# Optimization experiments

Measured on AMD Instinct MI355X. Metric: run time of the kernel, lower is better.

## Reference

```python
import jax, jax.numpy as jnp
import numpy as np
from jax import lax

T_DATA = 20000
E_NO = 2000
I_NO = 500
SUB_NO = 16
SYN_B = 3
HID = 256
T_SYN = 200
T_ENC = 80


def _causal_conv(x, kern):
    # x: [T, S] per-subunit drive; kern: [S, K] causal kernels (index = lag)
    S, K = kern.shape
    lhs = jnp.pad(x.T, ((0, 0), (K - 1, 0)))[None]        # [1, S, T+K-1]
    rhs = kern[:, ::-1][:, None, :]                        # flip then correlate == torch conv1d path
    out = lax.conv_general_dilated(lhs, rhs, (1,), 'VALID', feature_group_count=S)
    return out[0].T                                        # [T, S]


def setup_inputs() -> dict:
    key = jax.random.key(0)
    ks = jax.random.split(key, 16)
    V_in = jax.random.normal(ks[0], (T_DATA,), jnp.float32) * 5.0 - 69.0
    S_e = jax.random.bernoulli(ks[1], 0.02, (T_DATA, E_NO)).astype(jnp.float32)
    S_i = jax.random.bernoulli(ks[2], 0.02, (T_DATA, I_NO)).astype(jnp.float32)
    # synapse -> subunit one-hot assignment matrices [sub_no, n_syn]
    C_syn_e = jax.nn.one_hot(jax.random.randint(ks[3], (E_NO,), 0, SUB_NO), SUB_NO, dtype=jnp.float32).T
    C_syn_i = jax.nn.one_hot(jax.random.randint(ks[4], (I_NO,), 0, SUB_NO), SUB_NO, dtype=jnp.float32).T
    # parameters, initialized exactly as in __init__
    K_syn = jnp.stack([jnp.full((SUB_NO, SYN_B), 0.04),
                       jnp.full((SUB_NO, SYN_B), -0.02),
                       jnp.full((SUB_NO, SYN_B), 0.02)], axis=-1)          # [sub, B, 3]
    tau_syn = jnp.tile((jnp.arange(SYN_B, dtype=jnp.float32) + 1.6)[:, None], (1, 3))  # [B, 3]
    delta_syn = jnp.full((SUB_NO, 2), 2.0, jnp.float32)
    enc_bias = jnp.zeros((SUB_NO - 1,), jnp.float32)
    W_in = 2 * T_ENC - 1

    def lin(k, fan_out, fan_in):
        kw, kb = jax.random.split(k)
        s = 1.0 / np.sqrt(fan_in)
        return (jax.random.uniform(kw, (fan_out, fan_in), jnp.float32, -s, s),
                jax.random.uniform(kb, (fan_out,), jnp.float32, -s, s))

    W1, b1 = lin(ks[5], HID, W_in)
    W2, b2 = lin(ks[6], HID, HID)
    W3, b3 = lin(ks[7], HID, HID)
    W4, b4 = lin(ks[8], SUB_NO - 1, HID)
    a1 = jnp.float32(0.25)
    a2 = jnp.float32(0.25)
    a3 = jnp.float32(0.25)
    return dict(V_in=V_in, S_e=S_e, S_i=S_i, C_syn_e=C_syn_e, C_syn_i=C_syn_i,
                K_syn=K_syn, tau_syn=tau_syn, delta_syn=delta_syn, enc_bias=enc_bias,
                W1=W1, b1=b1, a1=a1, W2=W2, b2=b2, a2=a2, W3=W3, b3=b3, a3=a3,
                W4=W4, b4=b4)


def reference(V_in, S_e, S_i, C_syn_e, C_syn_i, K_syn, tau_syn, delta_syn, enc_bias,
              W1, b1, a1, W2, b2, a2, W3, b3, a3, W4, b4):
    T = V_in.shape[0]
    # ---- spike_convolve, fully vectorized over (subunit, basis) ----
    t = jnp.arange(T_SYN, dtype=V_in.dtype)                 # [T_syn]
    d = jnp.exp(delta_syn)                                   # [sub, 2]
    te = jnp.maximum(t[None, :] - d[:, 0:1], 0.0)            # [sub, T_syn]
    ti = jnp.maximum(t[None, :] - d[:, 1:2], 0.0)
    tau = jnp.exp(tau_syn)                                   # [B, 3]
    tte = te[:, None, :] / tau[None, :, 0, None]             # [sub, B, T_syn]
    tti = ti[:, None, :] / tau[None, :, 1, None]
    ker_e = jnp.einsum('sbt,sb->st', tte * jnp.exp(-tte), K_syn[:, :, 0])
    ker_i = jnp.einsum('sbt,sb->st', tti * jnp.exp(-tti), K_syn[:, :, 1])
    in_e = S_e @ C_syn_e.T                                   # [T, sub]
    in_i = S_i @ C_syn_i.T
    S_conv = _causal_conv(in_e, ker_e) + _causal_conv(in_i, ker_i)   # [T, sub]
    # ---- encode: batched sliding-window MLP (replaces per-timestep loop) ----
    W = 2 * T_ENC - 1
    Vpad = jnp.zeros((T + W,), V_in.dtype).at[T_ENC - 1:T_ENC - 1 + T].set(V_in)
    idx = jnp.arange(T)[:, None] + jnp.arange(W)[None, :]    # [T, W]
    win = Vpad[idx]                                          # [T, W]
    prelu = lambda x, a: jnp.where(x >= 0, x, a * x)
    h = prelu(win @ W1.T + b1, a1)
    h = prelu(h @ W2.T + b2, a2)
    h = prelu(h @ W3.T + b3, a3)
    nn_out = h @ W4.T + b4                                   # [T, sub-1]
    return jax.nn.sigmoid(nn_out + S_conv[:, 1:] + enc_bias)
```

## Files before the change

kernel.cpp:

```cpp
#include <hip/hip_runtime.h>
#include <cstdint>
#include <cstddef>

#define T_DATA 20000
#define E_NO 2000
#define I_NO 500
#define SUB_NO 16
#define HID 256
#define T_SYN 200
#define T_ENC 80
#define W_IN 159

typedef __attribute__((ext_vector_type(8))) __bf16 bf16x8;
typedef __attribute__((ext_vector_type(8))) short short8;
typedef __attribute__((ext_vector_type(4))) float floatx4;
typedef __attribute__((ext_vector_type(4))) unsigned int uint4v;
typedef __attribute__((ext_vector_type(2))) unsigned int uint2v;

__device__ __forceinline__ float bf2f(unsigned short u) {
    union { unsigned int i; float f; } v; v.i = ((unsigned int)u) << 16; return v.f;
}
__device__ __forceinline__ unsigned short f2bf(float f) {
    union { float f; unsigned int i; } v; v.f = f;
    unsigned int r = v.i + 0x7FFFu + ((v.i >> 16) & 1u);
    return (unsigned short)(r >> 16);
}
__device__ __forceinline__ float inload(const void* p, int i, int isbf) {
    return isbf ? bf2f(((const unsigned short*)p)[i]) : ((const float*)p)[i];
}

__device__ __forceinline__ int detect_bf(const void* Se, int* sfl) {
    if (threadIdx.x == 0) *sfl = 0;
    __syncthreads();
    const unsigned int* w = (const unsigned int*)Se;
    int la = 0;
    #pragma unroll
    for (int i = 0; i < 4; i++)
        la |= (w[i * 256 + threadIdx.x] & 0xFFFFu) ? 1 : 0;
    if (la) atomicOr(sfl, 1);
    __syncthreads();
    return *sfl;
}

#define OFF_KERE   16u
#define OFF_KERI   12816u
#define OFF_SHE    25616u
#define OFF_SHI    33616u
#define OFF_W1H    35616u
#define OFF_W1L    117536u
#define OFF_W2H    199456u
#define OFF_W2L    330528u
#define OFF_W3H    461600u
#define OFF_W3L    592672u
#define OFF_W4H    723744u
#define OFF_W4L    731424u
#define OFF_INE    739104u
#define OFF_INI    1059104u
#define OFF_SCONV  1379104u

__global__ void k_setup(const void* Se, const void* Ksyn, const void* tau_syn, const void* dly,
                        const void* Ce, const void* Ci,
                        const void* W1, const void* W2, const void* W3, const void* W4,
                        float* ker_e, float* ker_i, unsigned char* sh_e, unsigned char* sh_i,
                        unsigned short* W1h, unsigned short* W1l,
                        unsigned short* W2h, unsigned short* W2l,
                        unsigned short* W3h, unsigned short* W3l,
                        unsigned short* W4h, unsigned short* W4l) {
    __shared__ int sfl;
    int f = detect_bf(Se, &sfl);
    int id = blockIdx.x * 256 + threadIdx.x;
    if (id < 6400) {
        int c = id < 3200 ? 0 : 1;
        int q = id - c * 3200;
        int s = q / 200, j = q - s * 200;
        float d = expf(inload(dly, s * 2 + c, f));
        float tt = fmaxf((float)j - d, 0.0f);
        float acc = 0.f;
        #pragma unroll
        for (int b = 0; b < 3; b++) {
            float tau = expf(inload(tau_syn, b * 3 + c, f));
            float x = tt / tau;
            acc += x * expf(-x) * inload(Ksyn, (s * 3 + b) * 3 + c, f);
        }
        (c == 0 ? ker_e : ker_i)[s * 200 + j] = acc;
    } else if (id < 8400) {
        int e = id - 6400;
        int a = 0;
        for (int s = 0; s < 16; s++) if (inload(Ce, s * E_NO + e, f) > 0.5f) a = s;
        sh_e[e] = (unsigned char)(a * 8);
    } else if (id < 8900) {
        int e = id - 8400;
        int a = 0;
        for (int s = 0; s < 16; s++) if (inload(Ci, s * I_NO + e, f) > 0.5f) a = s;
        sh_i[e] = (unsigned char)(a * 8);
    } else if (id < 49860) {
        int q = id - 8900;
        int n = q / 160, k = q - n * 160;
        float v = (k < W_IN) ? inload(W1, n * W_IN + k, f) : 0.f;
        unsigned short hi = f2bf(v);
        W1h[q] = hi;
        W1l[q] = f2bf(v - bf2f(hi));
    } else if (id < 115396) {
        int q = id - 49860;
        float v = inload(W2, q, f);
        unsigned short hi = f2bf(v);
        W2h[q] = hi;
        W2l[q] = f2bf(v - bf2f(hi));
    } else if (id < 180932) {
        int q = id - 115396;
        float v = inload(W3, q, f);
        unsigned short hi = f2bf(v);
        W3h[q] = hi;
        W3l[q] = f2bf(v - bf2f(hi));
    } else if (id < 184772) {
        int q = id - 180932;
        float v = inload(W4, q, f);
        unsigned short hi = f2bf(v);
        W4h[q] = hi;
        W4l[q] = f2bf(v - bf2f(hi));
    }
}

__device__ __forceinline__ void acc_slot(unsigned int b, unsigned int sh,
                                         unsigned long long& lo, unsigned long long& hi) {
    unsigned int up = sh >> 6;
    unsigned int s6 = sh & 63;
    lo += (unsigned long long)(b & (up ^ 1u)) << s6;
    hi += (unsigned long long)(b & up) << s6;
}

__global__ void __launch_bounds__(256) k_spikes(const void* Se, const void* Si,
                         const unsigned char* sh_e, const unsigned char* sh_i,
                         unsigned char* in_e, unsigned char* in_i) {
    __shared__ int sfl;
    __shared__ __align__(8) unsigned char she[E_NO];
    __shared__ __align__(8) unsigned char shi[I_NO];
    for (int i = threadIdx.x; i < E_NO / 4; i += 256)
        ((unsigned int*)she)[i] = ((const unsigned int*)sh_e)[i];
    for (int i = threadIdx.x; i < I_NO / 4; i += 256)
        ((unsigned int*)shi)[i] = ((const unsigned int*)sh_i)[i];
    int f = detect_bf(Se, &sfl);
    int lane = threadIdx.x & 63;
    int wave = threadIdx.x >> 6;
    int t = blockIdx.x * 4 + wave;
    unsigned long long e0 = 0, e1 = 0, i0 = 0, i1 = 0;
    if (f) {
        const uint4v* re = (const uint4v*)((const unsigned short*)Se + (size_t)t * E_NO);
        #pragma unroll
        for (int it = 0; it < 4; it++) {
            int c = it * 64 + lane;
            if (c < 250) {
                uint4v v = re[c];
                unsigned long long q = *(const unsigned long long*)&she[c * 8];
                #pragma unroll
                for (int w = 0; w < 4; w++) {
                    unsigned int x = v[w];
                    acc_slot((x >> 7) & 1u,  (unsigned int)(q >> (16 * w)) & 0xFFu, e0, e1);
                    acc_slot((x >> 23) & 1u, (unsigned int)(q >> (16 * w + 8)) & 0xFFu, e0, e1);
                }
            }
        }
        const uint2v* ri = (const uint2v*)((const unsigned short*)Si + (size_t)t * I_NO);
        #pragma unroll
        for (int it = 0; it < 2; it++) {
            int c = it * 64 + lane;
            if (c < 125) {
                uint2v v = ri[c];
                unsigned int q = *(const unsigned int*)&shi[c * 4];
                #pragma unroll
                for (int w = 0; w < 2; w++) {
                    unsigned int x = v[w];
                    acc_slot((x >> 7) & 1u,  (q >> (16 * w)) & 0xFFu, i0, i1);
                    acc_slot((x >> 23) & 1u, (q >> (16 * w + 8)) & 0xFFu, i0, i1);
                }
            }
        }
    } else {
        const uint4v* re = (const uint4v*)((const float*)Se + (size_t)t * E_NO);
        #pragma unroll
        for (int it = 0; it < 8; it++) {
            int c = it * 64 + lane;
            if (c < 500) {
                uint4v v = re[c];
                unsigned int q = *(const unsigned int*)&she[c * 4];
                #pragma unroll
                for (int w = 0; w < 4; w++)
                    acc_slot((v[w] >> 23) & 1u, (q >> (8 * w)) & 0xFFu, e0, e1);
            }
        }
        const uint2v* ri = (const uint2v*)((const float*)Si + (size_t)t * I_NO);
        #pragma unroll
        for (int it = 0; it < 4; it++) {
            int c = it * 64 + lane;
            if (c < 250) {
                uint2v v = ri[c];
                unsigned int q = *(const unsigned short*)&shi[c * 2];
                #pragma unroll
                for (int w = 0; w < 2; w++)
                    acc_slot((v[w] >> 23) & 1u, (q >> (8 * w)) & 0xFFu, i0, i1);
            }
        }
    }
    for (int off = 32; off; off >>= 1) {
        e0 += __shfl_xor(e0, off);
        e1 += __shfl_xor(e1, off);
        i0 += __shfl_xor(i0, off);
        i1 += __shfl_xor(i1, off);
    }
    if (lane < 16) {
        unsigned long long a = (lane < 8) ? e0 : e1;
        in_e[(size_t)t * 16 + lane] = (unsigned char)((a >> ((lane & 7) * 8)) & 0xFF);
    } else if (lane < 32) {
        int s = lane - 16;
        unsigned long long a = (s < 8) ? i0 : i1;
        in_i[(size_t)t * 16 + s] = (unsigned char)((a >> ((s & 7) * 8)) & 0xFF);
    }
}

__global__ void __launch_bounds__(256) k_conv(
        const unsigned char* in_e, const unsigned char* in_i,
        const float* ker_e, const float* ker_i, float* S_conv) {
    __shared__ float se[263 * 17];
    __shared__ float si[263 * 17];
    __shared__ float ke[16 * 201];
    __shared__ float ki[16 * 201];
    int t0 = blockIdx.x * 64;
    for (int idx = threadIdx.x; idx < 263 * 4; idx += 256) {
        int r = idx >> 2, wi = idx & 3;
        int t = t0 - 199 + r;
        unsigned int ve = 0, vi = 0;
        if (t >= 0 && t < T_DATA) {
            ve = ((const unsigned int*)in_e)[t * 4 + wi];
            vi = ((const unsigned int*)in_i)[t * 4 + wi];
        }
        #pragma unroll
        for (int b = 0; b < 4; b++) {
            se[r * 17 + wi * 4 + b] = (float)((ve >> (8 * b)) & 0xFF);
            si[r * 17 + wi * 4 + b] = (float)((vi >> (8 * b)) & 0xFF);
        }
    }
    for (int idx = threadIdx.x; idx < 3200; idx += 256) {
        int s = idx / 200, j = idx - s * 200;
        ke[s * 201 + j] = ker_e[idx];
        ki[s * 201 + j] = ker_i[idx];
    }
    __syncthreads();
    int s = threadIdx.x & 15, g4 = (threadIdx.x >> 4) * 4;
    float a0 = 0.f, a1 = 0.f, a2 = 0.f, a3 = 0.f;
    float w0 = se[(g4 + 199) * 17 + s], w1 = se[(g4 + 200) * 17 + s];
    float w2 = se[(g4 + 201) * 17 + s], w3 = se[(g4 + 202) * 17 + s];
    float x0 = si[(g4 + 199) * 17 + s], x1 = si[(g4 + 200) * 17 + s];
    float x2 = si[(g4 + 201) * 17 + s], x3 = si[(g4 + 202) * 17 + s];
    #pragma unroll 4
    for (int j = 0; j < 200; j++) {
        float kej = ke[s * 201 + j];
        float kij = ki[s * 201 + j];
        a0 += w0 * kej + x0 * kij;
        a1 += w1 * kej + x1 * kij;
        a2 += w2 * kej + x2 * kij;
        a3 += w3 * kej + x3 * kij;
        int lr = g4 + 198 - j; lr = lr < 0 ? 0 : lr;
        float nw = se[lr * 17 + s], nx = si[lr * 17 + s];
        w3 = w2; w2 = w1; w1 = w0; w0 = nw;
        x3 = x2; x2 = x1; x1 = x0; x0 = nx;
    }
    int tb = t0 + g4;
    if (tb + 0 < T_DATA) S_conv[(size_t)(tb + 0) * 16 + s] = a0;
    if (tb + 1 < T_DATA) S_conv[(size_t)(tb + 1) * 16 + s] = a1;
    if (tb + 2 < T_DATA) S_conv[(size_t)(tb + 2) * 16 + s] = a2;
    if (tb + 3 < T_DATA) S_conv[(size_t)(tb + 3) * 16 + s] = a3;
}

template<bool BF>
__device__ __forceinline__ void mlp_body(
    const void* V,
    const unsigned short* W1h, const unsigned short* W1l, const void* b1, const void* a1p,
    const unsigned short* W2h, const unsigned short* W2l, const void* b2, const void* a2p,
    const unsigned short* W3h, const unsigned short* W3l, const void* b3, const void* a3p,
    const unsigned short* W4h, const unsigned short* W4l, const void* b4,
    const void* encb, const float* S_conv, void* out,
    unsigned short* Ahi, unsigned short* Alo)
{
    int tid = threadIdx.x;
    int lane = tid & 63, wave = tid >> 6;
    int lm = lane & 15, quad = lane >> 4;
    int t0 = blockIdx.x * 32;

    auto ld = [&](const void* p, int i) -> float {
        return BF ? bf2f(((const unsigned short*)p)[i]) : ((const float*)p)[i];
    };

    for (int idx = tid; idx < 32 * 160; idx += 256) {
        int m = idx / 160, k = idx - m * 160;
        int tg = t0 + m + k - (T_ENC - 1);
        float v = 0.f;
        if (k < W_IN && tg >= 0 && tg < T_DATA) v = ld(V, tg);
        unsigned short hi = f2bf(v);
        int col = (((k >> 3) ^ m) << 3) | (k & 7);
        Ahi[m * 256 + col] = hi;
        Alo[m * 256 + col] = f2bf(v - bf2f(hi));
    }
    __syncthreads();

    floatx4 acc[2][4];
    auto aoff = [&](int mt, int ks) {
        int arow = mt * 16 + lm;
        return arow * 256 + ((((ks << 2) | quad) ^ arow) << 3);
    };

    auto epi = [&](const void* bias, float alpha) {
        __syncthreads();
        #pragma unroll
        for (int mt = 0; mt < 2; mt++) {
            #pragma unroll
            for (int nt = 0; nt < 4; nt++) {
                int cn = wave * 64 + nt * 16 + lm;
                float bb = ld(bias, cn);
                #pragma unroll
                for (int j = 0; j < 4; j++) {
                    int row = mt * 16 + quad * 4 + j;
                    float h = acc[mt][nt][j] + bb;
                    h = (h >= 0.f) ? h : alpha * h;
                    unsigned short hi = f2bf(h);
                    int col = (((cn >> 3) ^ row) << 3) | (cn & 7);
                    Ahi[row * 256 + col] = hi;
                    Alo[row * 256 + col] = f2bf(h - bf2f(hi));
                }
            }
        }
        __syncthreads();
    };

    floatx4 z = {0.f, 0.f, 0.f, 0.f};
    {
        #pragma unroll
        for (int mt = 0; mt < 2; mt++)
            #pragma unroll
            for (int nt = 0; nt < 4; nt++) acc[mt][nt] = z;
        #pragma unroll
        for (int ks = 0; ks < 5; ks++) {
            bf16x8 ah0 = *(const bf16x8*)&Ahi[aoff(0, ks)];
            bf16x8 ah1 = *(const bf16x8*)&Ahi[aoff(1, ks)];
            bf16x8 al0, al1;
            if (!BF) { al0 = *(const bf16x8*)&Alo[aoff(0, ks)];
                       al1 = *(const bf16x8*)&Alo[aoff(1, ks)]; }
            #pragma unroll
            for (int nt = 0; nt < 4; nt++) {
                int cn = wave * 64 + nt * 16 + lm;
                size_t bo = (size_t)cn * 160 + ks * 32 + quad * 8;
                bf16x8 bh = *(const bf16x8*)(W1h + bo);
                acc[0][nt] = __builtin_amdgcn_mfma_f32_16x16x32_bf16(ah0, bh, acc[0][nt], 0, 0, 0);
                acc[1][nt] = __builtin_amdgcn_mfma_f32_16x16x32_bf16(ah1, bh, acc[1][nt], 0, 0, 0);
                if (!BF) {
                    bf16x8 bl = *(const bf16x8*)(W1l + bo);
                    acc[0][nt] = __builtin_amdgcn_mfma_f32_16x16x32_bf16(al0, bh, acc[0][nt], 0, 0, 0);
                    acc[1][nt] = __builtin_amdgcn_mfma_f32_16x16x32_bf16(al1, bh, acc[1][nt], 0, 0, 0);
                    acc[0][nt] = __builtin_amdgcn_mfma_f32_16x16x32_bf16(ah0, bl, acc[0][nt], 0, 0, 0);
                    acc[1][nt] = __builtin_amdgcn_mfma_f32_16x16x32_bf16(ah1, bl, acc[1][nt], 0, 0, 0);
                }
            }
        }
        epi(b1, ld(a1p, 0));
    }
    const unsigned short* Whs[2] = {W2h, W3h};
    const unsigned short* Wls[2] = {W2l, W3l};
    const void* bs[2] = {b2, b3};
    const void* as_[2] = {a2p, a3p};
    for (int l = 0; l < 2; l++) {
        #pragma unroll
        for (int mt = 0; mt < 2; mt++)
            #pragma unroll
            for (int nt = 0; nt < 4; nt++) acc[mt][nt] = z;
        const unsigned short* Wh = Whs[l];
        const unsigned short* Wl = Wls[l];
        #pragma unroll
        for (int ks = 0; ks < 8; ks++) {
            bf16x8 ah0 = *(const bf16x8*)&Ahi[aoff(0, ks)];
            bf16x8 ah1 = *(const bf16x8*)&Ahi[aoff(1, ks)];
            bf16x8 al0 = *(const bf16x8*)&Alo[aoff(0, ks)];
            bf16x8 al1 = *(const bf16x8*)&Alo[aoff(1, ks)];
            #pragma unroll
            for (int nt = 0; nt < 4; nt++) {
                int cn = wave * 64 + nt * 16 + lm;
                size_t bo = (size_t)cn * 256 + ks * 32 + quad * 8;
                bf16x8 bh = *(const bf16x8*)(Wh + bo);
                acc[0][nt] = __builtin_amdgcn_mfma_f32_16x16x32_bf16(ah0, bh, acc[0][nt], 0, 0, 0);
                acc[1][nt] = __builtin_amdgcn_mfma_f32_16x16x32_bf16(ah1, bh, acc[1][nt], 0, 0, 0);
                acc[0][nt] = __builtin_amdgcn_mfma_f32_16x16x32_bf16(al0, bh, acc[0][nt], 0, 0, 0);
                acc[1][nt] = __builtin_amdgcn_mfma_f32_16x16x32_bf16(al1, bh, acc[1][nt], 0, 0, 0);
                if (!BF) {
                    bf16x8 bl = *(const bf16x8*)(Wl + bo);
                    acc[0][nt] = __builtin_amdgcn_mfma_f32_16x16x32_bf16(ah0, bl, acc[0][nt], 0, 0, 0);
                    acc[1][nt] = __builtin_amdgcn_mfma_f32_16x16x32_bf16(ah1, bl, acc[1][nt], 0, 0, 0);
                }
            }
        }
        epi(bs[l], ld(as_[l], 0));
    }
    if (wave < 2) {
        int mt = wave;
        short8 z8 = {0, 0, 0, 0, 0, 0, 0, 0};
        bf16x8 bz = __builtin_bit_cast(bf16x8, z8);
        floatx4 a4 = z;
        #pragma unroll
        for (int ks = 0; ks < 8; ks++) {
            bf16x8 ah = *(const bf16x8*)&Ahi[aoff(mt, ks)];
            bf16x8 al = *(const bf16x8*)&Alo[aoff(mt, ks)];
            bf16x8 bh = bz, bl = bz;
            if (lm < 15) {
                size_t bo = (size_t)lm * 256 + ks * 32 + quad * 8;
                bh = *(const bf16x8*)(W4h + bo);
                if (!BF) bl = *(const bf16x8*)(W4l + bo);
            }
            a4 = __builtin_amdgcn_mfma_f32_16x16x32_bf16(ah, bh, a4, 0, 0, 0);
            a4 = __builtin_amdgcn_mfma_f32_16x16x32_bf16(al, bh, a4, 0, 0, 0);
            if (!BF)
                a4 = __builtin_amdgcn_mfma_f32_16x16x32_bf16(ah, bl, a4, 0, 0, 0);
        }
        if (lm < 15) {
            float bb = ld(b4, lm) + ld(encb, lm);
            #pragma unroll
            for (int j = 0; j < 4; j++) {
                int row = mt * 16 + quad * 4 + j;
                int t = t0 + row;
                float x = a4[j] + bb + S_conv[(size_t)t * 16 + lm + 1];
                x = fminf(fmaxf(x, -40.f), 40.f);
                float sg = 1.f / (1.f + expf(-x));
                if (BF) ((unsigned short*)out)[(size_t)t * 15 + lm] = f2bf(sg);
                else    ((float*)out)[(size_t)t * 15 + lm] = sg;
            }
        }
    }
}

__global__ void __launch_bounds__(256) k_mlp(
    const void* Se, const void* V,
    const unsigned short* W1h, const unsigned short* W1l, const void* b1, const void* a1p,
    const unsigned short* W2h, const unsigned short* W2l, const void* b2, const void* a2p,
    const unsigned short* W3h, const unsigned short* W3l, const void* b3, const void* a3p,
    const unsigned short* W4h, const unsigned short* W4l, const void* b4,
    const void* encb, const float* S_conv, void* out) {
    __shared__ __align__(16) unsigned short Ahi[32 * 256];
    __shared__ __align__(16) unsigned short Alo[32 * 256];
    __shared__ int sfl;
    int f = detect_bf(Se, &sfl);
    if (f)
        mlp_body<true>(V, W1h, W1l, b1, a1p, W2h, W2l, b2, a2p, W3h, W3l, b3, a3p,
                       W4h, W4l, b4, encb, S_conv, out, Ahi, Alo);
    else
        mlp_body<false>(V, W1h, W1l, b1, a1p, W2h, W2l, b2, a2p, W3h, W3l, b3, a3p,
                        W4h, W4l, b4, encb, S_conv, out, Ahi, Alo);
}

extern "C" void kernel_launch(void* const* d_in, const int* in_sizes, int n_in,
                              void* d_out, int out_size, void* d_ws, size_t ws_size,
                              hipStream_t stream) {
    const void* V    = d_in[0];
    const void* Se   = d_in[1];
    const void* Si   = d_in[2];
    const void* Ce   = d_in[3];
    const void* Ci   = d_in[4];
    const void* Ksyn = d_in[5];
    const void* tau  = d_in[6];
    const void* dly  = d_in[7];
    const void* encb = d_in[8];
    const void* W1   = d_in[9];
    const void* b1   = d_in[10];
    const void* a1   = d_in[11];
    const void* W2   = d_in[12];
    const void* b2   = d_in[13];
    const void* a2   = d_in[14];
    const void* W3   = d_in[15];
    const void* b3   = d_in[16];
    const void* a3   = d_in[17];
    const void* W4   = d_in[18];
    const void* b4   = d_in[19];

    char* w = (char*)d_ws;
    float* ker_e = (float*)(w + OFF_KERE);
    float* ker_i = (float*)(w + OFF_KERI);
    unsigned char* sh_e = (unsigned char*)(w + OFF_SHE);
    unsigned char* sh_i = (unsigned char*)(w + OFF_SHI);
    unsigned short* W1h = (unsigned short*)(w + OFF_W1H);
    unsigned short* W1l = (unsigned short*)(w + OFF_W1L);
    unsigned short* W2h = (unsigned short*)(w + OFF_W2H);
    unsigned short* W2l = (unsigned short*)(w + OFF_W2L);
    unsigned short* W3h = (unsigned short*)(w + OFF_W3H);
    unsigned short* W3l = (unsigned short*)(w + OFF_W3L);
    unsigned short* W4h = (unsigned short*)(w + OFF_W4H);
    unsigned short* W4l = (unsigned short*)(w + OFF_W4L);
    unsigned char* in_e = (unsigned char*)(w + OFF_INE);
    unsigned char* in_i = (unsigned char*)(w + OFF_INI);
    float* S_conv = (float*)(w + OFF_SCONV);

    k_setup<<<722, 256, 0, stream>>>(Se, Ksyn, tau, dly, Ce, Ci, W1, W2, W3, W4,
                                     ker_e, ker_i, sh_e, sh_i,
                                     W1h, W1l, W2h, W2l, W3h, W3l, W4h, W4l);
    k_spikes<<<5000, 256, 0, stream>>>(Se, Si, sh_e, sh_i, in_e, in_i);
    k_conv<<<313, 256, 0, stream>>>(in_e, in_i, ker_e, ker_i, S_conv);
    k_mlp<<<625, 256, 0, stream>>>(Se, V, W1h, W1l, b1, a1, W2h, W2l, b2, a2,
                                   W3h, W3l, b3, a3, W4h, W4l, b4,
                                   encb, S_conv, d_out);
}
```

Measured before the change: 392.4 us.

## Double MLP row tile to 64 per block and preload weight fragments in bf16 path

Each MLP block now handles 64 timesteps instead of 32, so every loaded weight fragment is reused across four M-tiles. Grid size is halved and LDS doubles. In the bf16 path all B fragments for a layer are held in registers, and the redundant lo-part MFMAs and Alo stores are removed. This cuts weight traffic and the extra split-precision work, but raises register pressure and lowers the block count, with launch_bounds(256,2) added to control occupancy.

```diff
diff --git a/kernel.cpp b/kernel.cpp
--- a/kernel.cpp
+++ b/kernel.cpp
@@ -284,34 +284,34 @@
     int tid = threadIdx.x;
     int lane = tid & 63, wave = tid >> 6;
     int lm = lane & 15, quad = lane >> 4;
-    int t0 = blockIdx.x * 32;
+    int t0 = blockIdx.x * 64;
 
     auto ld = [&](const void* p, int i) -> float {
         return BF ? bf2f(((const unsigned short*)p)[i]) : ((const float*)p)[i];
     };
 
-    for (int idx = tid; idx < 32 * 160; idx += 256) {
+    for (int idx = tid; idx < 64 * 160; idx += 256) {
         int m = idx / 160, k = idx - m * 160;
         int tg = t0 + m + k - (T_ENC - 1);
         float v = 0.f;
         if (k < W_IN && tg >= 0 && tg < T_DATA) v = ld(V, tg);
         unsigned short hi = f2bf(v);
-        int col = (((k >> 3) ^ m) << 3) | (k & 7);
+        int col = (((k >> 3) ^ (m & 31)) << 3) | (k & 7);
         Ahi[m * 256 + col] = hi;
-        Alo[m * 256 + col] = f2bf(v - bf2f(hi));
+        if (!BF) Alo[m * 256 + col] = f2bf(v - bf2f(hi));
     }
     __syncthreads();
 
-    floatx4 acc[2][4];
+    floatx4 acc[4][4];
     auto aoff = [&](int mt, int ks) {
         int arow = mt * 16 + lm;
-        return arow * 256 + ((((ks << 2) | quad) ^ arow) << 3);
+        return arow * 256 + ((((ks << 2) | quad) ^ (arow & 31)) << 3);
     };
 
     auto epi = [&](const void* bias, float alpha) {
         __syncthreads();
         #pragma unroll
-        for (int mt = 0; mt < 2; mt++) {
+        for (int mt = 0; mt < 4; mt++) {
             #pragma unroll
             for (int nt = 0; nt < 4; nt++) {
                 int cn = wave * 64 + nt * 16 + lm;
@@ -322,9 +322,9 @@
                     float h = acc[mt][nt][j] + bb;
                     h = (h >= 0.f) ? h : alpha * h;
                     unsigned short hi = f2bf(h);
-                    int col = (((cn >> 3) ^ row) << 3) | (cn & 7);
+                    int col = (((cn >> 3) ^ (row & 31)) << 3) | (cn & 7);
                     Ahi[row * 256 + col] = hi;
-                    Alo[row * 256 + col] = f2bf(h - bf2f(hi));
+                    if (!BF) Alo[row * 256 + col] = f2bf(h - bf2f(hi));
                 }
             }
         }
@@ -334,29 +334,46 @@
     floatx4 z = {0.f, 0.f, 0.f, 0.f};
     {
         #pragma unroll
-        for (int mt = 0; mt < 2; mt++)
+        for (int mt = 0; mt < 4; mt++)
             #pragma unroll
             for (int nt = 0; nt < 4; nt++) acc[mt][nt] = z;
-        #pragma unroll
-        for (int ks = 0; ks < 5; ks++) {
-            bf16x8 ah0 = *(const bf16x8*)&Ahi[aoff(0, ks)];
-            bf16x8 ah1 = *(const bf16x8*)&Ahi[aoff(1, ks)];
-            bf16x8 al0, al1;
-            if (!BF) { al0 = *(const bf16x8*)&Alo[aoff(0, ks)];
-                       al1 = *(const bf16x8*)&Alo[aoff(1, ks)]; }
-            #pragma unroll
-            for (int nt = 0; nt < 4; nt++) {
-                int cn = wave * 64 + nt * 16 + lm;
-                size_t bo = (size_t)cn * 160 + ks * 32 + quad * 8;
-                bf16x8 bh = *(const bf16x8*)(W1h + bo);
-                acc[0][nt] = __builtin_amdgcn_mfma_f32_16x16x32_bf16(ah0, bh, acc[0][nt], 0, 0, 0);
-                acc[1][nt] = __builtin_amdgcn_mfma_f32_16x16x32_bf16(ah1, bh, acc[1][nt], 0, 0, 0);
-                if (!BF) {
+        if (BF) {
+            bf16x8 Bh[5][4];
+            #pragma unroll
+            for (int ks = 0; ks < 5; ks++)
+                #pragma unroll
+                for (int nt = 0; nt < 4; nt++)
+                    Bh[ks][nt] = *(const bf16x8*)(W1h + (size_t)(wave * 64 + nt * 16 + lm) * 160 + ks * 32 + quad * 8);
+            #pragma unroll
+            for (int ks = 0; ks < 5; ks++) {
+                bf16x8 a[4];
+                #pragma unroll
+                for (int mt = 0; mt < 4; mt++) a[mt] = *(const bf16x8*)&Ahi[aoff(mt, ks)];
+                #pragma unroll
+                for (int nt = 0; nt < 4; nt++)
+                    #pragma unroll
+                    for (int mt = 0; mt < 4; mt++)
+                        acc[mt][nt] = __builtin_amdgcn_mfma_f32_16x16x32_bf16(a[mt], Bh[ks][nt], acc[mt][nt], 0, 0, 0);
+            }
+        } else {
+            for (int ks = 0; ks < 5; ks++) {
+                bf16x8 ah[4], al[4];
+                #pragma unroll
+                for (int mt = 0; mt < 4; mt++) {
+                    ah[mt] = *(const bf16x8*)&Ahi[aoff(mt, ks)];
+                    al[mt] = *(const bf16x8*)&Alo[aoff(mt, ks)];
+                }
+                #pragma unroll
+                for (int nt = 0; nt < 4; nt++) {
+                    size_t bo = (size_t)(wave * 64 + nt * 16 + lm) * 160 + ks * 32 + quad * 8;
+                    bf16x8 bh = *(const bf16x8*)(W1h + bo);
                     bf16x8 bl = *(const bf16x8*)(W1l + bo);
-                    acc[0][nt] = __builtin_amdgcn_mfma_f32_16x16x32_bf16(al0, bh, acc[0][nt], 0, 0, 0);
-                    acc[1][nt] = __builtin_amdgcn_mfma_f32_16x16x32_bf16(al1, bh, acc[1][nt], 0, 0, 0);
-                    acc[0][nt] = __builtin_amdgcn_mfma_f32_16x16x32_bf16(ah0, bl, acc[0][nt], 0, 0, 0);
-                    acc[1][nt] = __builtin_amdgcn_mfma_f32_16x16x32_bf16(ah1, bl, acc[1][nt], 0, 0, 0);
+                    #pragma unroll
+                    for (int mt = 0; mt < 4; mt++) {
+                        acc[mt][nt] = __builtin_amdgcn_mfma_f32_16x16x32_bf16(ah[mt], bh, acc[mt][nt], 0, 0, 0);
+                        acc[mt][nt] = __builtin_amdgcn_mfma_f32_16x16x32_bf16(al[mt], bh, acc[mt][nt], 0, 0, 0);
+                        acc[mt][nt] = __builtin_amdgcn_mfma_f32_16x16x32_bf16(ah[mt], bl, acc[mt][nt], 0, 0, 0);
+                    }
                 }
             }
         }
@@ -368,36 +385,54 @@
     const void* as_[2] = {a2p, a3p};
     for (int l = 0; l < 2; l++) {
         #pragma unroll
-        for (int mt = 0; mt < 2; mt++)
+        for (int mt = 0; mt < 4; mt++)
             #pragma unroll
             for (int nt = 0; nt < 4; nt++) acc[mt][nt] = z;
         const unsigned short* Wh = Whs[l];
         const unsigned short* Wl = Wls[l];
-        #pragma unroll
-        for (int ks = 0; ks < 8; ks++) {
-            bf16x8 ah0 = *(const bf16x8*)&Ahi[aoff(0, ks)];
-            bf16x8 ah1 = *(const bf16x8*)&Ahi[aoff(1, ks)];
-            bf16x8 al0 = *(const bf16x8*)&Alo[aoff(0, ks)];
-            bf16x8 al1 = *(const bf16x8*)&Alo[aoff(1, ks)];
-            #pragma unroll
-            for (int nt = 0; nt < 4; nt++) {
-                int cn = wave * 64 + nt * 16 + lm;
-                size_t bo = (size_t)cn * 256 + ks * 32 + quad * 8;
-                bf16x8 bh = *(const bf16x8*)(Wh + bo);
-                acc[0][nt] = __builtin_amdgcn_mfma_f32_16x16x32_bf16(ah0, bh, acc[0][nt], 0, 0, 0);
-                acc[1][nt] = __builtin_amdgcn_mfma_f32_16x16x32_bf16(ah1, bh, acc[1][nt], 0, 0, 0);
-                acc[0][nt] = __builtin_amdgcn_mfma_f32_16x16x32_bf16(al0, bh, acc[0][nt], 0, 0, 0);
-                acc[1][nt] = __builtin_amdgcn_mfma_f32_16x16x32_bf16(al1, bh, acc[1][nt], 0, 0, 0);
-                if (!BF) {
+        if (BF) {
+            bf16x8 Bh[8][4];
+            #pragma unroll
+            for (int ks = 0; ks < 8; ks++)
+                #pragma unroll
+                for (int nt = 0; nt < 4; nt++)
+                    Bh[ks][nt] = *(const bf16x8*)(Wh + (size_t)(wave * 64 + nt * 16 + lm) * 256 + ks * 32 + quad * 8);
+            #pragma unroll
+            for (int ks = 0; ks < 8; ks++) {
+                bf16x8 a[4];
+                #pragma unroll
+                for (int mt = 0; mt < 4; mt++) a[mt] = *(const bf16x8*)&Ahi[aoff(mt, ks)];
+                #pragma unroll
+                for (int nt = 0; nt < 4; nt++)
+                    #pragma unroll
+                    for (int mt = 0; mt < 4; mt++)
+                        acc[mt][nt] = __builtin_amdgcn_mfma_f32_16x16x32_bf16(a[mt], Bh[ks][nt], acc[mt][nt], 0, 0, 0);
+            }
+        } else {
+            for (int ks = 0; ks < 8; ks++) {
+                bf16x8 ah[4], al[4];
+                #pragma unroll
+                for (int mt = 0; mt < 4; mt++) {
+                    ah[mt] = *(const bf16x8*)&Ahi[aoff(mt, ks)];
+                    al[mt] = *(const bf16x8*)&Alo[aoff(mt, ks)];
+                }
+                #pragma unroll
+                for (int nt = 0; nt < 4; nt++) {
+                    size_t bo = (size_t)(wave * 64 + nt * 16 + lm) * 256 + ks * 32 + quad * 8;
+                    bf16x8 bh = *(const bf16x8*)(Wh + bo);
                     bf16x8 bl = *(const bf16x8*)(Wl + bo);
-                    acc[0][nt] = __builtin_amdgcn_mfma_f32_16x16x32_bf16(ah0, bl, acc[0][nt], 0, 0, 0);
-                    acc[1][nt] = __builtin_amdgcn_mfma_f32_16x16x32_bf16(ah1, bl, acc[1][nt], 0, 0, 0);
+                    #pragma unroll
+                    for (int mt = 0; mt < 4; mt++) {
+                        acc[mt][nt] = __builtin_amdgcn_mfma_f32_16x16x32_bf16(ah[mt], bh, acc[mt][nt], 0, 0, 0);
+                        acc[mt][nt] = __builtin_amdgcn_mfma_f32_16x16x32_bf16(al[mt], bh, acc[mt][nt], 0, 0, 0);
+                        acc[mt][nt] = __builtin_amdgcn_mfma_f32_16x16x32_bf16(ah[mt], bl, acc[mt][nt], 0, 0, 0);
+                    }
                 }
             }
         }
         epi(bs[l], ld(as_[l], 0));
     }
-    if (wave < 2) {
+    {
         int mt = wave;
         short8 z8 = {0, 0, 0, 0, 0, 0, 0, 0};
         bf16x8 bz = __builtin_bit_cast(bf16x8, z8);
@@ -405,17 +440,18 @@
         #pragma unroll
         for (int ks = 0; ks < 8; ks++) {
             bf16x8 ah = *(const bf16x8*)&Ahi[aoff(mt, ks)];
-            bf16x8 al = *(const bf16x8*)&Alo[aoff(mt, ks)];
-            bf16x8 bh = bz, bl = bz;
-            if (lm < 15) {
-                size_t bo = (size_t)lm * 256 + ks * 32 + quad * 8;
-                bh = *(const bf16x8*)(W4h + bo);
-                if (!BF) bl = *(const bf16x8*)(W4l + bo);
-            }
+            bf16x8 bh = bz;
+            if (lm < 15)
+                bh = *(const bf16x8*)(W4h + (size_t)lm * 256 + ks * 32 + quad * 8);
             a4 = __builtin_amdgcn_mfma_f32_16x16x32_bf16(ah, bh, a4, 0, 0, 0);
-            a4 = __builtin_amdgcn_mfma_f32_16x16x32_bf16(al, bh, a4, 0, 0, 0);
-            if (!BF)
+            if (!BF) {
+                bf16x8 al = *(const bf16x8*)&Alo[aoff(mt, ks)];
+                bf16x8 bl = bz;
+                if (lm < 15)
+                    bl = *(const bf16x8*)(W4l + (size_t)lm * 256 + ks * 32 + quad * 8);
+                a4 = __builtin_amdgcn_mfma_f32_16x16x32_bf16(al, bh, a4, 0, 0, 0);
                 a4 = __builtin_amdgcn_mfma_f32_16x16x32_bf16(ah, bl, a4, 0, 0, 0);
+            }
         }
         if (lm < 15) {
             float bb = ld(b4, lm) + ld(encb, lm);
@@ -423,25 +459,27 @@
             for (int j = 0; j < 4; j++) {
                 int row = mt * 16 + quad * 4 + j;
                 int t = t0 + row;
-                float x = a4[j] + bb + S_conv[(size_t)t * 16 + lm + 1];
-                x = fminf(fmaxf(x, -40.f), 40.f);
-                float sg = 1.f / (1.f + expf(-x));
-                if (BF) ((unsigned short*)out)[(size_t)t * 15 + lm] = f2bf(sg);
-                else    ((float*)out)[(size_t)t * 15 + lm] = sg;
-            }
-        }
-    }
-}
-
-__global__ void __launch_bounds__(256) k_mlp(
+                if (t < T_DATA) {
+                    float x = a4[j] + bb + S_conv[(size_t)t * 16 + lm + 1];
+                    x = fminf(fmaxf(x, -40.f), 40.f);
+                    float sg = 1.f / (1.f + expf(-x));
+                    if (BF) ((unsigned short*)out)[(size_t)t * 15 + lm] = f2bf(sg);
+                    else    ((float*)out)[(size_t)t * 15 + lm] = sg;
+                }
+            }
+        }
+    }
+}
+
+__global__ void __launch_bounds__(256, 2) k_mlp(
     const void* Se, const void* V,
     const unsigned short* W1h, const unsigned short* W1l, const void* b1, const void* a1p,
     const unsigned short* W2h, const unsigned short* W2l, const void* b2, const void* a2p,
     const unsigned short* W3h, const unsigned short* W3l, const void* b3, const void* a3p,
     const unsigned short* W4h, const unsigned short* W4l, const void* b4,
     const void* encb, const float* S_conv, void* out) {
-    __shared__ __align__(16) unsigned short Ahi[32 * 256];
-    __shared__ __align__(16) unsigned short Alo[32 * 256];
+    __shared__ __align__(16) unsigned short Ahi[64 * 256];
+    __shared__ __align__(16) unsigned short Alo[64 * 256];
     __shared__ int sfl;
     int f = detect_bf(Se, &sfl);
     if (f)
@@ -498,7 +536,7 @@
                                      W1h, W1l, W2h, W2l, W3h, W3l, W4h, W4l);
     k_spikes<<<5000, 256, 0, stream>>>(Se, Si, sh_e, sh_i, in_e, in_i);
     k_conv<<<313, 256, 0, stream>>>(in_e, in_i, ker_e, ker_i, S_conv);
-    k_mlp<<<625, 256, 0, stream>>>(Se, V, W1h, W1l, b1, a1, W2h, W2l, b2, a2,
+    k_mlp<<<313, 256, 0, stream>>>(Se, V, W1h, W1l, b1, a1, W2h, W2l, b2, a2,
                                    W3h, W3l, b3, a3, W4h, W4l, b4,
                                    encb, S_conv, d_out);
 }
```

Measured after the change: 373.2 us. -4.9%, faster.
